# Kernel optimization log

Measured on AMD Instinct MI355X. Metric: run time of the kernel, lower is better.

Reference implementation:

```python
import jax, jax.numpy as jnp
import numpy as np
import math

D_MODEL = 1024
NUM_HEADS = 16
D_K = D_MODEL // NUM_HEADS


def setup_inputs() -> dict:
    key = jax.random.key(0)
    ks = jax.random.split(key, 5)
    scale = 1.0 / math.sqrt(D_MODEL)
    x = jax.random.normal(ks[0], (2, 2048, D_MODEL), dtype=jnp.float32)
    qkv_w = jax.random.uniform(ks[1], (3 * D_MODEL, D_MODEL), jnp.float32, -scale, scale)
    qkv_b = jax.random.uniform(ks[2], (3 * D_MODEL,), jnp.float32, -scale, scale)
    out_w = jax.random.uniform(ks[3], (D_MODEL, D_MODEL), jnp.float32, -scale, scale)
    out_b = jax.random.uniform(ks[4], (D_MODEL,), jnp.float32, -scale, scale)
    return {"x": x, "qkv_w": qkv_w, "qkv_b": qkv_b, "out_w": out_w, "out_b": out_b}


def reference(x, qkv_w, qkv_b, out_w, out_b):
    B, N, D = x.shape
    # fused QKV projection (torch Linear: x @ W.T + b)
    qkv = x @ qkv_w.T + qkv_b                       # (B, N, 3D)
    qkv = qkv.reshape(B, N, 3, NUM_HEADS, D_K)
    qkv = jnp.transpose(qkv, (2, 0, 3, 1, 4))        # (3, B, H, N, d_k)
    q, k, v = qkv[0], qkv[1], qkv[2]
    attn = jnp.einsum('bhnd,bhmd->bhnm', q, k) / math.sqrt(D_K)  # (B,H,N,N)
    attn = jax.nn.softmax(attn, axis=-1)
    out = jnp.einsum('bhnm,bhmd->bhnd', attn, v)     # (B,H,N,d_k)
    out = jnp.transpose(out, (0, 2, 1, 3)).reshape(B, N, D)
    return out @ out_w.T + out_b
```

## Files before the change

kernel.cpp:

```cpp
#include <hip/hip_runtime.h>
#include <hip/hip_bf16.h>


typedef __bf16 bf16x8 __attribute__((ext_vector_type(8)));
typedef __bf16 bf16x4 __attribute__((ext_vector_type(4)));
typedef short short4v __attribute__((ext_vector_type(4)));
typedef float f32x4 __attribute__((ext_vector_type(4)));

#define QSCALE 0.18033688011112042f

__device__ __forceinline__ unsigned short bfbits(float f) {
    union { __bf16 h; unsigned short u; } cv;
    cv.h = (__bf16)f;
    return cv.u;
}

__device__ __forceinline__ f32x4 mfma16(bf16x4 a, bf16x4 b, f32x4 c) {
#if __has_builtin(__builtin_amdgcn_mfma_f32_16x16x16bf16_1k)
    union { bf16x4 h; short4v s; } ua, ub;
    ua.h = a; ub.h = b;
    return __builtin_amdgcn_mfma_f32_16x16x16bf16_1k(ua.s, ub.s, c, 0, 0, 0);
#else
    f32x4 d = c;
    asm volatile("v_mfma_f32_16x16x16_bf16 %0, %1, %2, %0"
                 : "+v"(d) : "v"(a), "v"(b));
    return d;
#endif
}

__device__ __forceinline__ void gl_lds16(const void* g, void* l) {
    __builtin_amdgcn_global_load_lds(
        (__attribute__((address_space(1))) const unsigned int*)g,
        (__attribute__((address_space(3))) unsigned int*)l, 16, 0, 0);
}

__global__ void cvt_all(const float4* __restrict__ x,
                        const float4* __restrict__ wq,
                        const float4* __restrict__ wo,
                        ushort4* __restrict__ dst) {
    int i = blockIdx.x * blockDim.x + threadIdx.x;
    const int stride = gridDim.x * blockDim.x;
    for (; i < 2097152; i += stride) {
        float4 f;
        if (i < 1048576)       f = x[i];
        else if (i < 1835008)  f = wq[i - 1048576];
        else                   f = wo[i - 1835008];
        ushort4 o;
        o.x = bfbits(f.x); o.y = bfbits(f.y); o.z = bfbits(f.z); o.w = bfbits(f.w);
        dst[i] = o;
    }
}

template<int MODE>
__global__ __launch_bounds__(256, 3) void gemm_mfma(
    const unsigned short* __restrict__ A,
    const unsigned short* __restrict__ W,
    const float* __restrict__ bias,
    unsigned short* __restrict__ qo,
    unsigned short* __restrict__ ko,
    unsigned short* __restrict__ vto,
    float* __restrict__ fo) {
    __shared__ __attribute__((aligned(128))) unsigned char smem[32768];
    const int lane = threadIdx.x & 63;
    const int w = threadIdx.x >> 6;
    const int g = lane >> 4, c = lane & 15;
    const int wr = w >> 1, wc = w & 1;
    const int row0 = blockIdx.x * 128;
    const int col0 = blockIdx.y * 128;

    const int rloc = lane >> 3;
    const int csrc = ((lane & 7) ^ rloc) * 8;

    f32x4 acc[4][4] = {};

    for (int kt = 0; kt < 1024; kt += 64) {
        #pragma unroll
        for (int i = 0; i < 4; ++i) {
            const int r = i * 32 + w * 8 + rloc;
            gl_lds16(A + (size_t)(row0 + r) * 1024 + kt + csrc,
                     smem + i * 4096 + w * 1024);
            gl_lds16(W + (size_t)(col0 + r) * 1024 + kt + csrc,
                     smem + 16384 + i * 4096 + w * 1024);
        }
        __syncthreads();

        #pragma unroll
        for (int ks = 0; ks < 2; ++ks) {
            bf16x8 a[4], b[4];
            #pragma unroll
            for (int mi = 0; mi < 4; ++mi) {
                const int r = wr * 64 + mi * 16 + c;
                a[mi] = *(const bf16x8*)(smem + r * 128 + (((ks * 4 + g) ^ (r & 7)) * 16));
            }
            #pragma unroll
            for (int ni = 0; ni < 4; ++ni) {
                const int r = wc * 64 + ni * 16 + c;
                b[ni] = *(const bf16x8*)(smem + 16384 + r * 128 + (((ks * 4 + g) ^ (r & 7)) * 16));
            }
            #pragma unroll
            for (int mi = 0; mi < 4; ++mi)
                #pragma unroll
                for (int ni = 0; ni < 4; ++ni)
                    acc[mi][ni] = __builtin_amdgcn_mfma_f32_16x16x32_bf16(
                        a[mi], b[ni], acc[mi][ni], 0, 0, 0);
        }
        __syncthreads();
    }

    #pragma unroll
    for (int mi = 0; mi < 4; ++mi) {
        #pragma unroll
        for (int ni = 0; ni < 4; ++ni) {
            const int col = col0 + wc * 64 + ni * 16 + c;
            const float bv = bias[col];
            #pragma unroll
            for (int j = 0; j < 4; ++j) {
                const int row = row0 + wr * 64 + mi * 16 + 4 * g + j;
                float v = acc[mi][ni][j] + bv;
                if (MODE == 1) {
                    fo[(size_t)row * 1024 + col] = v;
                } else {
                    const int sec = col >> 10;
                    const int d = col & 1023;
                    const int h = d >> 6, dk = d & 63;
                    const int b_ = row >> 11, n = row & 2047;
                    const int bh = b_ * 16 + h;
                    if (sec == 0)
                        qo[((size_t)(bh * 2048 + n) << 6) + dk] = bfbits(v * QSCALE);
                    else if (sec == 1)
                        ko[((size_t)(bh * 2048 + n) << 6) + dk] = bfbits(v);
                    else
                        vto[(size_t)(bh * 64 + dk) * 2048 + n] = bfbits(v);
                }
            }
        }
    }
}

__global__ __launch_bounds__(128, 2) void attn_flash(
    const unsigned short* __restrict__ Q,
    const unsigned short* __restrict__ K,
    const unsigned short* __restrict__ Vt,
    unsigned short* __restrict__ O) {
    __shared__ __attribute__((aligned(128))) unsigned char smem[32768];
    const int lane = threadIdx.x & 63;
    const int w = threadIdx.x >> 6;
    const int g = lane >> 4, c = lane & 15;
    const int c7 = c & 7;
    const int bh = blockIdx.y;
    const int q0 = blockIdx.x * 64 + w * 32;
    const unsigned short* Qb = Q + (size_t)bh * 2048 * 64;
    const unsigned short* Kb = K + (size_t)bh * 2048 * 64;
    const unsigned short* Vb = Vt + (size_t)bh * 64 * 2048;

    const int rloc = lane >> 3;
    const int csrc = ((lane & 7) ^ (rloc & 7)) * 8;

    const int chunkKV0 = ((0 + g) ^ c7) * 16;
    const int chunkKV1 = ((4 + g) ^ c7) * 16;
    const int ghalf = (g >> 1);
    const int gsub = (g & 1) * 8;

    bf16x8 aq[2][2];
    #pragma unroll
    for (int qg = 0; qg < 2; ++qg)
        #pragma unroll
        for (int ks = 0; ks < 2; ++ks)
            aq[qg][ks] = *(const bf16x8*)(Qb + (size_t)(q0 + qg * 16 + c) * 64 + ks * 32 + 8 * g);

    f32x4 oa[4] = {}, ob[4] = {};
    f32x4 la = {}, lb = {};
    float ma = -1e30f, mb = -1e30f;

    bf16x4 ones4;
    #pragma unroll
    for (int i = 0; i < 4; ++i) ones4[i] = (__bf16)1.0f;

    #pragma unroll
    for (int tt = 0; tt < 4; ++tt) {
        const int t = 4 * w + tt;
        const int row = 8 * t + rloc;
        gl_lds16(Kb + (size_t)row * 64 + csrc, smem + t * 1024);
        gl_lds16(Vb + (size_t)row * 2048 + csrc, smem + 16384 + t * 1024);
    }
    __syncthreads();

    int cur = 0;
    for (int kv = 0; kv < 2048; kv += 64) {
        if (kv + 64 < 2048) {
            const int nb = cur ^ 1;
            #pragma unroll
            for (int tt = 0; tt < 4; ++tt) {
                const int t = 4 * w + tt;
                const int row = 8 * t + rloc;
                gl_lds16(Kb + (size_t)(kv + 64 + row) * 64 + csrc,
                         smem + nb * 8192 + t * 1024);
                gl_lds16(Vb + (size_t)row * 2048 + (kv + 64) + csrc,
                         smem + 16384 + nb * 8192 + t * 1024);
            }
        }

        const unsigned char* Kt = smem + cur * 8192;
        const unsigned char* Vtb = smem + 16384 + cur * 8192;

        f32x4 sa[4] = {}, sb[4] = {};
        __builtin_amdgcn_s_setprio(1);
        #pragma unroll
        for (int nj = 0; nj < 4; ++nj) {
            bf16x8 bk0 = *(const bf16x8*)(Kt + nj * 2048 + c * 128 + chunkKV0);
            bf16x8 bk1 = *(const bf16x8*)(Kt + nj * 2048 + c * 128 + chunkKV1);
            sa[nj] = __builtin_amdgcn_mfma_f32_16x16x32_bf16(bk0, aq[0][0], sa[nj], 0, 0, 0);
            sa[nj] = __builtin_amdgcn_mfma_f32_16x16x32_bf16(bk1, aq[0][1], sa[nj], 0, 0, 0);
            sb[nj] = __builtin_amdgcn_mfma_f32_16x16x32_bf16(bk0, aq[1][0], sb[nj], 0, 0, 0);
            sb[nj] = __builtin_amdgcn_mfma_f32_16x16x32_bf16(bk1, aq[1][1], sb[nj], 0, 0, 0);
        }
        __builtin_amdgcn_s_setprio(0);

        float pa = sa[0][0], pb = sb[0][0];
        #pragma unroll
        for (int nj = 0; nj < 4; ++nj)
            #pragma unroll
            for (int j = 0; j < 4; ++j) {
                pa = fmaxf(pa, sa[nj][j]);
                pb = fmaxf(pb, sb[nj][j]);
            }

        const bool trig = (pa > ma + 8.f) || (pb > mb + 8.f);
        if (__any((int)trig)) {
            float rm = pa;
            rm = fmaxf(rm, __shfl_xor(rm, 16));
            rm = fmaxf(rm, __shfl_xor(rm, 32));
            float mnew = fmaxf(ma, rm);
            float sc = __builtin_amdgcn_exp2f(ma - mnew);
            ma = mnew;
            #pragma unroll
            for (int j = 0; j < 4; ++j) {
                const float scj = __shfl(sc, 4 * g + j);
                la[j] *= scj;
                #pragma unroll
                for (int ni = 0; ni < 4; ++ni) oa[ni][j] *= scj;
            }
            rm = pb;
            rm = fmaxf(rm, __shfl_xor(rm, 16));
            rm = fmaxf(rm, __shfl_xor(rm, 32));
            mnew = fmaxf(mb, rm);
            sc = __builtin_amdgcn_exp2f(mb - mnew);
            mb = mnew;
            #pragma unroll
            for (int j = 0; j < 4; ++j) {
                const float scj = __shfl(sc, 4 * g + j);
                lb[j] *= scj;
                #pragma unroll
                for (int ni = 0; ni < 4; ++ni) ob[ni][j] *= scj;
            }
        }

        bf16x4 qa_[4], qb_[4];
        #pragma unroll
        for (int nj = 0; nj < 4; ++nj)
            #pragma unroll
            for (int j = 0; j < 4; ++j) {
                qa_[nj][j] = (__bf16)__builtin_amdgcn_exp2f(sa[nj][j] - ma);
                qb_[nj][j] = (__bf16)__builtin_amdgcn_exp2f(sb[nj][j] - mb);
            }

        f32x4 lta = {}, ltb = {};
        __builtin_amdgcn_s_setprio(1);
        #pragma unroll
        for (int nj = 0; nj < 4; ++nj) {
            lta = mfma16(qa_[nj], ones4, lta);
            ltb = mfma16(qb_[nj], ones4, ltb);
            #pragma unroll
            for (int ni = 0; ni < 4; ++ni) {
                bf16x4 bv = *(const bf16x4*)(Vtb + (ni * 16 + c) * 128 +
                                             (((2 * nj + ghalf) ^ c7) * 16) + gsub);
                oa[ni] = mfma16(qa_[nj], bv, oa[ni]);
                ob[ni] = mfma16(qb_[nj], bv, ob[ni]);
            }
        }
        __builtin_amdgcn_s_setprio(0);
        la += lta;
        lb += ltb;

        __syncthreads();
        cur ^= 1;
    }

    const int b_ = bh >> 4, h = bh & 15;
    #pragma unroll
    for (int ni = 0; ni < 4; ++ni) {
        #pragma unroll
        for (int j = 0; j < 4; ++j) {
            const int col = h * 64 + ni * 16 + c;
            const int rowa = b_ * 2048 + q0 + 4 * g + j;
            O[(size_t)rowa * 1024 + col] = bfbits(oa[ni][j] / la[j]);
            const int rowb = rowa + 16;
            O[(size_t)rowb * 1024 + col] = bfbits(ob[ni][j] / lb[j]);
        }
    }
}

extern "C" void kernel_launch(void* const* d_in, const int* in_sizes, int n_in,
                              void* d_out, int out_size, void* d_ws, size_t ws_size,
                              hipStream_t stream) {
    const float* x     = (const float*)d_in[0];
    const float* qkv_w = (const float*)d_in[1];
    const float* qkv_b = (const float*)d_in[2];
    const float* out_w = (const float*)d_in[3];
    const float* out_b = (const float*)d_in[4];
    float* out = (float*)d_out;

    char* ws = (char*)d_ws;
    unsigned short* xb   = (unsigned short*)(ws);
    unsigned short* wqkv = (unsigned short*)(ws + (8u  << 20));
    unsigned short* wout = (unsigned short*)(ws + (14u << 20));
    unsigned short* qb   = (unsigned short*)(ws + (16u << 20));
    unsigned short* kb   = (unsigned short*)(ws + (24u << 20));
    unsigned short* vtb  = (unsigned short*)(ws + (32u << 20));

    cvt_all<<<2048, 256, 0, stream>>>((const float4*)x, (const float4*)qkv_w,
                                      (const float4*)out_w, (ushort4*)ws);

    gemm_mfma<0><<<dim3(32, 24), 256, 0, stream>>>(xb, wqkv, qkv_b, qb, kb, vtb, nullptr);

    unsigned short* ao = xb;
    attn_flash<<<dim3(32, 32), 128, 0, stream>>>(qb, kb, vtb, ao);

    gemm_mfma<1><<<dim3(32, 8), 256, 0, stream>>>(ao, wout, out_b, nullptr, nullptr, nullptr, out);
}
```

Baseline: 130.5 us.

## Split attention over KV halves with a merge kernel and larger blocks

Attention now splits the 2048-key range into two halves along a new grid z dimension. Each block uses 4 waves covering 128 queries, and each half writes its normalized partial output together with its row max and row sum. A new merge kernel combines the two partials with softmax rescaling before the output projection. This is meant to raise parallelism and occupancy for attention, at the cost of extra global traffic for the partials, an extra launch, and a second bf16 rounding of the output.

```diff
diff --git a/kernel.cpp b/kernel.cpp
--- a/kernel.cpp
+++ b/kernel.cpp
@@ -13,6 +13,12 @@
     union { __bf16 h; unsigned short u; } cv;
     cv.h = (__bf16)f;
     return cv.u;
+}
+
+__device__ __forceinline__ float bf2f(unsigned short u) {
+    union { unsigned int i; float f; } v;
+    v.i = ((unsigned int)u) << 16;
+    return v.f;
 }
 
 __device__ __forceinline__ f32x4 mfma16(bf16x4 a, bf16x4 b, f32x4 c) {
@@ -37,17 +43,21 @@
 __global__ void cvt_all(const float4* __restrict__ x,
                         const float4* __restrict__ wq,
                         const float4* __restrict__ wo,
-                        ushort4* __restrict__ dst) {
+                        ushort4* __restrict__ d0,
+                        ushort4* __restrict__ d1,
+                        ushort4* __restrict__ d2) {
     int i = blockIdx.x * blockDim.x + threadIdx.x;
     const int stride = gridDim.x * blockDim.x;
     for (; i < 2097152; i += stride) {
         float4 f;
-        if (i < 1048576)       f = x[i];
-        else if (i < 1835008)  f = wq[i - 1048576];
-        else                   f = wo[i - 1835008];
+        ushort4* d;
+        int k;
+        if (i < 1048576)       { f = x[i];           d = d0; k = i; }
+        else if (i < 1835008)  { f = wq[i - 1048576]; d = d1; k = i - 1048576; }
+        else                   { f = wo[i - 1835008]; d = d2; k = i - 1835008; }
         ushort4 o;
         o.x = bfbits(f.x); o.y = bfbits(f.y); o.z = bfbits(f.z); o.w = bfbits(f.w);
-        dst[i] = o;
+        d[k] = o;
     }
 }
 
@@ -137,18 +147,21 @@
     }
 }
 
-__global__ __launch_bounds__(128, 2) void attn_flash(
+__global__ __launch_bounds__(256, 4) void attn_flash(
     const unsigned short* __restrict__ Q,
     const unsigned short* __restrict__ K,
     const unsigned short* __restrict__ Vt,
-    unsigned short* __restrict__ O) {
+    unsigned short* __restrict__ Pout,
+    float* __restrict__ Mb,
+    float* __restrict__ Lb) {
     __shared__ __attribute__((aligned(128))) unsigned char smem[32768];
     const int lane = threadIdx.x & 63;
     const int w = threadIdx.x >> 6;
     const int g = lane >> 4, c = lane & 15;
     const int c7 = c & 7;
     const int bh = blockIdx.y;
-    const int q0 = blockIdx.x * 64 + w * 32;
+    const int hz = blockIdx.z;
+    const int q0 = blockIdx.x * 128 + w * 32;
     const unsigned short* Qb = Q + (size_t)bh * 2048 * 64;
     const unsigned short* Kb = K + (size_t)bh * 2048 * 64;
     const unsigned short* Vb = Vt + (size_t)bh * 64 * 2048;
@@ -158,7 +171,7 @@
 
     const int chunkKV0 = ((0 + g) ^ c7) * 16;
     const int chunkKV1 = ((4 + g) ^ c7) * 16;
-    const int ghalf = (g >> 1);
+    const int ghalf = g >> 1;
     const int gsub = (g & 1) * 8;
 
     bf16x8 aq[2][2];
@@ -176,27 +189,30 @@
     #pragma unroll
     for (int i = 0; i < 4; ++i) ones4[i] = (__bf16)1.0f;
 
-    #pragma unroll
-    for (int tt = 0; tt < 4; ++tt) {
-        const int t = 4 * w + tt;
+    const int gt0 = hz * 16;
+
+    #pragma unroll
+    for (int tt = 0; tt < 2; ++tt) {
+        const int t = 2 * w + tt;
         const int row = 8 * t + rloc;
-        gl_lds16(Kb + (size_t)row * 64 + csrc, smem + t * 1024);
-        gl_lds16(Vb + (size_t)row * 2048 + csrc, smem + 16384 + t * 1024);
+        gl_lds16(Kb + (size_t)(gt0 * 64 + row) * 64 + csrc, smem + t * 1024);
+        gl_lds16(Vb + (size_t)row * 2048 + gt0 * 64 + csrc, smem + 16384 + t * 1024);
     }
     __syncthreads();
 
-    int cur = 0;
-    for (int kv = 0; kv < 2048; kv += 64) {
-        if (kv + 64 < 2048) {
+    for (int t = 0; t < 16; ++t) {
+        const int cur = t & 1;
+        if (t + 1 < 16) {
             const int nb = cur ^ 1;
-            #pragma unroll
-            for (int tt = 0; tt < 4; ++tt) {
-                const int t = 4 * w + tt;
-                const int row = 8 * t + rloc;
-                gl_lds16(Kb + (size_t)(kv + 64 + row) * 64 + csrc,
-                         smem + nb * 8192 + t * 1024);
-                gl_lds16(Vb + (size_t)row * 2048 + (kv + 64) + csrc,
-                         smem + 16384 + nb * 8192 + t * 1024);
+            const int gt = gt0 + t + 1;
+            #pragma unroll
+            for (int tt = 0; tt < 2; ++tt) {
+                const int ti = 2 * w + tt;
+                const int row = 8 * ti + rloc;
+                gl_lds16(Kb + (size_t)(gt * 64 + row) * 64 + csrc,
+                         smem + nb * 8192 + ti * 1024);
+                gl_lds16(Vb + (size_t)row * 2048 + gt * 64 + csrc,
+                         smem + 16384 + nb * 8192 + ti * 1024);
             }
         }
 
@@ -283,20 +299,59 @@
         lb += ltb;
 
         __syncthreads();
-        cur ^= 1;
     }
 
     const int b_ = bh >> 4, h = bh & 15;
+    unsigned short* Pp = Pout + (size_t)hz * 4194304;
     #pragma unroll
     for (int ni = 0; ni < 4; ++ni) {
         #pragma unroll
         for (int j = 0; j < 4; ++j) {
             const int col = h * 64 + ni * 16 + c;
             const int rowa = b_ * 2048 + q0 + 4 * g + j;
-            O[(size_t)rowa * 1024 + col] = bfbits(oa[ni][j] / la[j]);
-            const int rowb = rowa + 16;
-            O[(size_t)rowb * 1024 + col] = bfbits(ob[ni][j] / lb[j]);
-        }
+            Pp[(size_t)rowa * 1024 + col] = bfbits(oa[ni][j] / la[j]);
+            Pp[(size_t)(rowa + 16) * 1024 + col] = bfbits(ob[ni][j] / lb[j]);
+        }
+    }
+    const int mlbase = (hz * 32 + bh) * 2048 + q0;
+    if (g == 0) {
+        Mb[mlbase + c] = ma;
+        Mb[mlbase + 16 + c] = mb;
+    }
+    if (c == 0) {
+        #pragma unroll
+        for (int j = 0; j < 4; ++j) {
+            Lb[mlbase + 4 * g + j] = la[j];
+            Lb[mlbase + 16 + 4 * g + j] = lb[j];
+        }
+    }
+}
+
+__global__ __launch_bounds__(256) void attn_merge(const float* __restrict__ Mb,
+                                                  const float* __restrict__ Lb,
+                                                  unsigned short* __restrict__ P) {
+    const unsigned tid = blockIdx.x * 256 + threadIdx.x;
+    const unsigned base = tid * 8;
+    const int r = base >> 10, col = base & 1023;
+    const int bh = ((r >> 11) << 4) + (col >> 6);
+    const int i0 = bh * 2048 + (r & 2047);
+    const float m0 = Mb[i0], m1 = Mb[65536 + i0];
+    const float l0 = Lb[i0], l1 = Lb[65536 + i0];
+    const float mx = fmaxf(m0, m1);
+    float w0 = l0 * __builtin_amdgcn_exp2f(m0 - mx);
+    float w1 = l1 * __builtin_amdgcn_exp2f(m1 - mx);
+    const float inv = 1.f / (w0 + w1);
+    w0 *= inv; w1 *= inv;
+    ushort4* p0 = (ushort4*)(P + (size_t)r * 1024 + col);
+    const ushort4* p1 = (const ushort4*)(P + 4194304 + (size_t)r * 1024 + col);
+    #pragma unroll
+    for (int k = 0; k < 2; ++k) {
+        ushort4 a = p0[k], b = p1[k], o;
+        o.x = bfbits(w0 * bf2f(a.x) + w1 * bf2f(b.x));
+        o.y = bfbits(w0 * bf2f(a.y) + w1 * bf2f(b.y));
+        o.z = bfbits(w0 * bf2f(a.z) + w1 * bf2f(b.z));
+        o.w = bfbits(w0 * bf2f(a.w) + w1 * bf2f(b.w));
+        p0[k] = o;
     }
 }
 
@@ -313,18 +368,23 @@
     char* ws = (char*)d_ws;
     unsigned short* xb   = (unsigned short*)(ws);
     unsigned short* wqkv = (unsigned short*)(ws + (8u  << 20));
-    unsigned short* wout = (unsigned short*)(ws + (14u << 20));
     unsigned short* qb   = (unsigned short*)(ws + (16u << 20));
     unsigned short* kb   = (unsigned short*)(ws + (24u << 20));
     unsigned short* vtb  = (unsigned short*)(ws + (32u << 20));
+    unsigned short* wout = (unsigned short*)(ws + (40u << 20));
+    float* Mb = (float*)(ws + (42u << 20));
+    float* Lb = (float*)(ws + (42u << 20) + (512u << 10));
 
     cvt_all<<<2048, 256, 0, stream>>>((const float4*)x, (const float4*)qkv_w,
-                                      (const float4*)out_w, (ushort4*)ws);
+                                      (const float4*)out_w,
+                                      (ushort4*)xb, (ushort4*)wqkv, (ushort4*)wout);
 
     gemm_mfma<0><<<dim3(32, 24), 256, 0, stream>>>(xb, wqkv, qkv_b, qb, kb, vtb, nullptr);
 
-    unsigned short* ao = xb;
-    attn_flash<<<dim3(32, 32), 128, 0, stream>>>(qb, kb, vtb, ao);
-
-    gemm_mfma<1><<<dim3(32, 8), 256, 0, stream>>>(ao, wout, out_b, nullptr, nullptr, nullptr, out);
-}
+    unsigned short* part = xb;
+    attn_flash<<<dim3(16, 32, 2), 256, 0, stream>>>(qb, kb, vtb, part, Mb, Lb);
+
+    attn_merge<<<2048, 256, 0, stream>>>(Mb, Lb, part);
+
+    gemm_mfma<1><<<dim3(32, 8), 256, 0, stream>>>(part, wout, out_b, nullptr, nullptr, nullptr, out);
+}
```

New measurement: 127.2 us. -2.5%, faster.
